# Kernel optimization log

Measured on AMD Instinct MI355X. Metric: run time of the kernel, lower is better.

## Reference

```python
import jax, jax.numpy as jnp
import numpy as np

D = 1024
H = 16
DH = D // H  # 64


def setup_inputs() -> dict:
    key = jax.random.key(0)
    ks = jax.random.split(key, 7)
    X = jax.random.normal(ks[0], (2, 2048, D), dtype=jnp.float32)
    # Per-head projection weights stacked along head axis: [H, D, DH]
    s = 1.0 / np.sqrt(D)
    Wq = jax.random.uniform(ks[1], (H, D, DH), jnp.float32, -s, s)
    Wk = jax.random.uniform(ks[2], (H, D, DH), jnp.float32, -s, s)
    Wv = jax.random.uniform(ks[3], (H, D, DH), jnp.float32, -s, s)
    bq = jax.random.uniform(ks[4], (H, DH), jnp.float32, -s, s)
    bk = jax.random.uniform(ks[5], (H, DH), jnp.float32, -s, s)
    bv = jax.random.uniform(ks[6], (H, DH), jnp.float32, -s, s)
    return {"X": X, "Wq": Wq, "bq": bq, "Wk": Wk, "bk": bk, "Wv": Wv, "bv": bv}


def reference(X, Wq, bq, Wk, bk, Wv, bv):
    B, S, _ = X.shape
    # Per-head linear projections (batched over heads): [B, H, S, DH]
    Q = jnp.einsum('bsd,hde->bhse', X, Wq) + bq[None, :, None, :]
    K = jnp.einsum('bsd,hde->bhse', X, Wk) + bk[None, :, None, :]
    V = jnp.einsum('bsd,hde->bhse', X, Wv) + bv[None, :, None, :]
    scale = jnp.sqrt(jnp.asarray(DH, dtype=X.dtype))
    QK = jnp.einsum('bhse,bhte->bhst', Q, K) / scale  # [B, H, S, S]
    # Faithful to source: softmax over full row FIRST, then lower-tri mask
    # (post-softmax tril, no renormalization).
    sQK = jax.nn.softmax(QK, axis=-1)
    tril = jnp.tril(jnp.ones((S, S), dtype=X.dtype))
    sQK = sQK * tril
    out = jnp.einsum('bhst,bhte->bhse', sQK, V)  # [B, H, S, DH]
    # Concatenate heads along feature dim (torch.cat over per-head outputs)
    return out.transpose(0, 2, 1, 3).reshape(B, S, H * DH)
```

## Files before the change

### kernel.cpp

```cpp
#include <hip/hip_runtime.h>
#include <math.h>

#define B_  2
#define S_  2048
#define D_  1024
#define H_  16
#define DH_ 64

typedef unsigned short u16;
typedef unsigned int   u32;
typedef _Float16       f16;
typedef _Float16 half8  __attribute__((ext_vector_type(8)));
typedef _Float16 half4  __attribute__((ext_vector_type(4)));
typedef float    f32x4  __attribute__((ext_vector_type(4)));

#if __has_builtin(__builtin_amdgcn_exp2f)
#define EXP2(x) __builtin_amdgcn_exp2f(x)
#else
#define EXP2(x) exp2f(x)
#endif

__device__ __forceinline__ u16 h_bits(f16 h){ return __builtin_bit_cast(u16, h); }

__global__ __launch_bounds__(256) void prep_kernel(
    const float* __restrict__ X,
    const float* __restrict__ Wq, const float* __restrict__ Wk,
    const float* __restrict__ Wv,
    u16* __restrict__ Xhi, u16* __restrict__ Xlo, u16* __restrict__ Wt)
{
    __shared__ float Wf[64][65];
    const int bid = blockIdx.x;
    const int c   = threadIdx.x;

    if (bid < 4096){
        const int idx = bid * 256 + c;
        float4 v = ((const float4*)X)[idx];
        float fv[4] = {v.x, v.y, v.z, v.w};
        u16 hh[4], ll[4];
        #pragma unroll
        for (int j = 0; j < 4; ++j){
            f16 hi = (f16)fv[j];
            hh[j] = h_bits(hi);
            ll[j] = h_bits((f16)(fv[j] - (float)hi));
        }
        uint2 ph, pl;
        ph.x = hh[0] | ((u32)hh[1] << 16);
        ph.y = hh[2] | ((u32)hh[3] << 16);
        pl.x = ll[0] | ((u32)ll[1] << 16);
        pl.y = ll[2] | ((u32)ll[3] << 16);
        ((uint2*)Xhi)[idx] = ph;
        ((uint2*)Xlo)[idx] = pl;
        return;
    }

    const int wb = bid - 4096;
    const int d0 = (wb & 15) * 64;
    const int h  = (wb >> 4) & 15;
    const int which = wb >> 8;
    const float* src = (which == 0) ? Wq : (which == 1) ? Wk : Wv;
    src += (size_t)h * D_ * DH_;

    #pragma unroll
    for (int it = 0; it < 4; ++it){
        int d  = (c >> 4) + 16 * it;
        int e4 = (c & 15) * 4;
        float4 v = *(const float4*)(src + (size_t)(d0 + d) * DH_ + e4);
        Wf[d][e4+0] = v.x; Wf[d][e4+1] = v.y; Wf[d][e4+2] = v.z; Wf[d][e4+3] = v.w;
    }
    __syncthreads();
    u16* dst = Wt + (size_t)(which * H_ + h) * DH_ * D_;
    #pragma unroll
    for (int it = 0; it < 4; ++it){
        int e  = (c >> 4) + 16 * it;
        int d4 = (c & 15) * 4;
        u16 q[4];
        #pragma unroll
        for (int j = 0; j < 4; ++j)
            q[j] = h_bits((f16)(Wf[d4 + j][e] * 64.0f));
        u32* p = (u32*)(dst + (size_t)e * D_ + d0 + d4);
        p[0] = q[0] | ((u32)q[1] << 16);
        p[1] = q[2] | ((u32)q[3] << 16);
    }
}

__device__ __forceinline__ void gload16(const void* g, void* l){
    __builtin_amdgcn_global_load_lds(
        (const __attribute__((address_space(1))) void*)g,
        (__attribute__((address_space(3))) void*)l, 16, 0, 0);
}

__device__ __forceinline__ half8 frag16(const char* hb, int row, int quad){
    int off = row * 64 + ((quad * 16) ^ ((row & 6) << 3));
    return __builtin_bit_cast(half8, *(const uint4*)(hb + off));
}

#define FENCE() asm volatile("" ::: "memory")
#define BARX()  do{ FENCE(); __builtin_amdgcn_s_barrier(); FENCE(); }while(0)
#define WAIT_VM4() asm volatile("s_waitcnt vmcnt(4)" ::: "memory")
#define WAIT_VM0() asm volatile("s_waitcnt vmcnt(0)" ::: "memory")

#define STAGE_A(t_, kh_) do{ \
    const int _t = (t_); \
    const int _gk = ((_t & 15) << 6) + ((kh_) << 5); \
    const u16* _g0 = ((_t < 16) ? xa0h : xa0l) + _gk; \
    const u16* _g1 = ((_t < 16) ? xa1h : xa1l) + _gk; \
    char* _l = AsB + ((_t & 1) << 15) + ((kh_) << 14); \
    gload16(_g0, _l + ldw0); \
    gload16(_g1, _l + ldw1); \
}while(0)

#define STAGE_B(t_, kh_) do{ \
    const int _t = (t_); \
    const int _gk = ((_t & 15) << 6) + ((kh_) << 5); \
    char* _l = BsB + ((_t & 1) << 15) + ((kh_) << 14); \
    gload16(wb0 + _gk, _l + ldw0); \
    gload16(wb1 + _gk, _l + ldw1); \
}while(0)

#define READ_B(bh_) do{ \
    _Pragma("unroll") \
    for (int nf_ = 0; nf_ < 4; ++nf_) \
        bfr[nf_] = frag16((bh_), wn * 64 + nf_ * 16 + ln, quad); \
}while(0)

#define READ_A(ah_, mbase_) do{ \
    _Pragma("unroll") \
    for (int mi_ = 0; mi_ < 4; ++mi_) \
        af[mi_] = frag16((ah_), wm * 128 + ((mbase_) + mi_) * 16 + ln, quad); \
}while(0)

#define MFMA_BLOCK(mbase_) do{ \
    BARX(); \
    asm volatile("s_waitcnt lgkmcnt(0)" ::: "memory"); \
    __builtin_amdgcn_sched_barrier(0); \
    __builtin_amdgcn_s_setprio(1); \
    _Pragma("unroll") \
    for (int mi_ = 0; mi_ < 4; ++mi_){ \
        _Pragma("unroll") \
        for (int nf_ = 0; nf_ < 4; ++nf_) \
            acc[(mbase_) + mi_][nf_] = __builtin_amdgcn_mfma_f32_16x16x32_f16( \
                af[mi_], bfr[nf_], acc[(mbase_) + mi_][nf_], 0, 0, 0); \
    } \
    __builtin_amdgcn_s_setprio(0); \
}while(0)

__global__ __launch_bounds__(512, 2) void proj_kernel(
    const u16* __restrict__ Xhi, const u16* __restrict__ Xlo,
    const u16* __restrict__ Wt,
    const float* __restrict__ bq, const float* __restrict__ bk,
    const float* __restrict__ bv,
    f16* __restrict__ Qh, f16* __restrict__ Kh, f16* __restrict__ Vt)
{
    __shared__ __align__(16) char AsB[65536];
    __shared__ __align__(16) char BsB[65536];

    const int tid  = threadIdx.x;
    const int lane = tid & 63;
    const int w    = tid >> 6;
    const int wm   = w >> 2;
    const int wn   = w & 3;
    const int quad = lane >> 4;
    const int ln   = lane & 15;

    const int bid = blockIdx.x;
    const int swz = (bid & 7) * 24 + (bid >> 3);
    const int m0  = (swz / 12) * 256;
    const int c0  = (swz % 12) * 256;

    const int Lr0 = w * 1024 + lane * 16;
    const int Lr1 = (8 + w) * 1024 + lane * 16;
    const int P0  = Lr0 ^ (((Lr0 >> 7) & 3) << 4);
    const int P1  = Lr1 ^ (((Lr1 >> 7) & 3) << 4);
    const int row0 = P0 >> 6,        row1 = P1 >> 6;
    const int ko0  = (P0 & 63) >> 1, ko1  = (P1 & 63) >> 1;

    const u16* xa0h = Xhi + (size_t)(m0 + row0) * D_ + ko0;
    const u16* xa1h = Xhi + (size_t)(m0 + row1) * D_ + ko1;
    const u16* xa0l = Xlo + (size_t)(m0 + row0) * D_ + ko0;
    const u16* xa1l = Xlo + (size_t)(m0 + row1) * D_ + ko1;
    const u16* wb0  = Wt  + (size_t)(c0 + row0) * D_ + ko0;
    const u16* wb1  = Wt  + (size_t)(c0 + row1) * D_ + ko1;

    const int ldw0 = w * 1024;
    const int ldw1 = (8 + w) * 1024;

    f32x4 acc[8][4];
    #pragma unroll
    for (int i = 0; i < 8; ++i)
        #pragma unroll
        for (int j = 0; j < 4; ++j)
            acc[i][j] = (f32x4){0.f, 0.f, 0.f, 0.f};

    STAGE_A(0, 0); STAGE_B(0, 0); STAGE_A(0, 1); STAGE_B(0, 1);
    STAGE_A(1, 0); STAGE_B(1, 0);
    WAIT_VM4();
    BARX();

    half8 bfr[4], af[4];

    #pragma unroll 2
    for (int t = 0; t < 32; ++t){
        const char* Ah = AsB + ((t & 1) << 15);
        const char* Bh = BsB + ((t & 1) << 15);

        READ_B(Bh); READ_A(Ah, 0);
        if (t < 31) STAGE_A(t + 1, 1);
        MFMA_BLOCK(0);
        BARX();

        READ_A(Ah, 4);
        if (t < 31) STAGE_B(t + 1, 1);
        MFMA_BLOCK(4);
        BARX();

        READ_B(Bh + 16384); READ_A(Ah + 16384, 0);
        if (t < 30) STAGE_A(t + 2, 0);
        MFMA_BLOCK(0);
        BARX();

        READ_A(Ah + 16384, 4);
        if (t < 30) STAGE_B(t + 2, 0);
        MFMA_BLOCK(4);
        if (t < 30) { WAIT_VM4(); } else { WAIT_VM0(); }
        BARX();
    }

    const float QSCALE = 0.125f * 1.44269504088896340736f;
    const float INV64  = 0.015625f;
    #pragma unroll
    for (int nf = 0; nf < 4; ++nf){
        int colg  = c0 + wn * 64 + nf * 16 + ln;
        int which = colg >> 10;
        int h     = (colg >> 6) & 15;
        int e     = colg & 63;
        const float* bp = (which == 0) ? bq : (which == 1) ? bk : bv;
        float bias = bp[h * DH_ + e];
        if (which < 2){
            f16* op = (which == 0) ? Qh : Kh;
            float scale = (which == 0) ? QSCALE : 1.0f;
            #pragma unroll
            for (int mf = 0; mf < 8; ++mf)
                #pragma unroll
                for (int r = 0; r < 4; ++r){
                    int sg = m0 + wm * 128 + mf * 16 + 4 * quad + r;
                    int b  = sg >> 11;
                    int s  = sg & (S_ - 1);
                    float val = (acc[mf][nf][r] * INV64 + bias) * scale;
                    op[((size_t)(b * H_ + h) * S_ + s) * DH_ + e] = (f16)val;
                }
        } else {
            #pragma unroll
            for (int mf = 0; mf < 8; ++mf){
                int sg0 = m0 + wm * 128 + mf * 16 + 4 * quad;
                int b   = sg0 >> 11;
                int s0  = sg0 & (S_ - 1);
                u16 p[4];
                #pragma unroll
                for (int r = 0; r < 4; ++r)
                    p[r] = h_bits((f16)(acc[mf][nf][r] * INV64 + bias));
                uint2 pk;
                pk.x = p[0] | ((u32)p[1] << 16);
                pk.y = p[2] | ((u32)p[3] << 16);
                *(uint2*)((u16*)Vt + ((size_t)((b * H_ + h) * DH_ + e)) * S_ + s0) = pk;
            }
        }
    }
}

#define AKS 72

__global__ __launch_bounds__(256, 4) void attn_kernel(
    const f16* __restrict__ Qh, const f16* __restrict__ Kh,
    const f16* __restrict__ Vt, float* __restrict__ Out)
{
    __shared__ u16 Ks[64 * AKS];
    __shared__ u16 Vs[64 * AKS];

    const int tid  = threadIdx.x;
    const int lane = tid & 63;
    const int w    = tid >> 6;
    const int quad = lane >> 4;
    const int ln   = lane & 15;
    const int hb   = blockIdx.x;
    const int i    = blockIdx.y;
    const int h    = hb & 15;
    const int b    = hb >> 4;
    const int bh   = hb;
    const int sub  = w & 1;
    const int qbase = (w >> 1) ? (S_ - 32 * (i + 1) + 16 * sub)
                               : (32 * i + 16 * sub);
    const int vmax  = S_ - 32 * i - 1;

    const u16* Qg = (const u16*)Qh + (size_t)bh * S_ * DH_;
    const u16* Kg = (const u16*)Kh + (size_t)bh * S_ * DH_;
    const u16* Vg = (const u16*)Vt + (size_t)bh * DH_ * S_;

    half8 qf[2];
    #pragma unroll
    for (int ks = 0; ks < 2; ++ks)
        qf[ks] = __builtin_bit_cast(half8,
            *(const uint4*)(Qg + (size_t)(qbase + ln) * DH_ + 32 * ks + 8 * quad));

    const int kr = tid >> 3;
    const int kc = (tid & 7) * 8;

    uint4 kA = *(const uint4*)(Kg + (size_t)kr * DH_ + kc);
    uint4 kB = *(const uint4*)(Kg + (size_t)(kr + 32) * DH_ + kc);
    uint4 vA = *(const uint4*)(Vg + (size_t)kr * S_ + kc);
    uint4 vB = *(const uint4*)(Vg + (size_t)(kr + 32) * S_ + kc);

    float l_r = 0.f;
    f32x4 o_acc[4];
    #pragma unroll
    for (int nt = 0; nt < 4; ++nt) o_acc[nt] = (f32x4){0.f, 0.f, 0.f, 0.f};

    const int qrow   = qbase + ln;
    const int pv_lim = qbase + 15;

    for (int t0 = 0; t0 < S_; t0 += 64){
        __syncthreads();
        *(uint4*)&Ks[kr * AKS + kc]        = kA;
        *(uint4*)&Ks[(kr + 32) * AKS + kc] = kB;
        if (t0 <= vmax){
            *(uint4*)&Vs[kr * AKS + kc]        = vA;
            *(uint4*)&Vs[(kr + 32) * AKS + kc] = vB;
        }
        const int tn = t0 + 64;
        if (tn < S_){
            kA = *(const uint4*)(Kg + (size_t)(tn + kr) * DH_ + kc);
            kB = *(const uint4*)(Kg + (size_t)(tn + kr + 32) * DH_ + kc);
            if (tn <= vmax){
                vA = *(const uint4*)(Vg + (size_t)kr * S_ + tn + kc);
                vB = *(const uint4*)(Vg + (size_t)(kr + 32) * S_ + tn + kc);
            }
        }
        __syncthreads();

        f32x4 sc[4];
        #pragma unroll
        for (int mt = 0; mt < 4; ++mt) sc[mt] = (f32x4){0.f, 0.f, 0.f, 0.f};
        #pragma unroll
        for (int ks = 0; ks < 2; ++ks)
            #pragma unroll
            for (int mt = 0; mt < 4; ++mt){
                half8 kf = __builtin_bit_cast(half8,
                    *(const uint4*)&Ks[(16 * mt + ln) * AKS + 32 * ks + 8 * quad]);
                sc[mt] = __builtin_amdgcn_mfma_f32_16x16x32_f16(kf, qf[ks], sc[mt], 0, 0, 0);
            }

        #pragma unroll
        for (int mt = 0; mt < 4; ++mt)
            #pragma unroll
            for (int r = 0; r < 4; ++r)
                sc[mt][r] = EXP2(sc[mt][r]);
        float s = ((sc[0][0] + sc[0][1] + sc[0][2] + sc[0][3]) +
                   (sc[1][0] + sc[1][1] + sc[1][2] + sc[1][3])) +
                  ((sc[2][0] + sc[2][1] + sc[2][2] + sc[2][3]) +
                   (sc[3][0] + sc[3][1] + sc[3][2] + sc[3][3]));
        s += __shfl_xor(s, 16);
        s += __shfl_xor(s, 32);
        l_r += s;

        #pragma unroll
        for (int mt = 0; mt < 4; ++mt){
            const int ts = t0 + 16 * mt;
            if (ts <= pv_lim){
                half4 pf;
                if (ts == qbase){
                    int tb = ts + 4 * quad;
                    #pragma unroll
                    for (int r = 0; r < 4; ++r)
                        pf[r] = (tb + r > qrow) ? (f16)0.f : (f16)sc[mt][r];
                } else {
                    #pragma unroll
                    for (int r = 0; r < 4; ++r)
                        pf[r] = (f16)sc[mt][r];
                }
                #pragma unroll
                for (int nt = 0; nt < 4; ++nt){
                    half4 vf = __builtin_bit_cast(half4,
                        *(const uint2*)&Vs[(16 * nt + ln) * AKS + 16 * mt + 4 * quad]);
                    o_acc[nt] = __builtin_amdgcn_mfma_f32_16x16x16f16(pf, vf, o_acc[nt], 0, 0, 0);
                }
            }
        }
    }

    #pragma unroll
    for (int r = 0; r < 4; ++r){
        float lv  = __shfl(l_r, (lane & 48) | (4 * quad + r));
        float inv = 1.0f / lv;
        int sg = qbase + 4 * quad + r;
        float* op = Out + ((size_t)b * S_ + sg) * D_ + h * DH_;
        #pragma unroll
        for (int nt = 0; nt < 4; ++nt)
            op[16 * nt + ln] = o_acc[nt][r] * inv;
    }
}

extern "C" void kernel_launch(void* const* d_in, const int* in_sizes, int n_in,
                              void* d_out, int out_size, void* d_ws, size_t ws_size,
                              hipStream_t stream)
{
    const float* X  = (const float*)d_in[0];
    const float* Wq = (const float*)d_in[1];
    const float* bq = (const float*)d_in[2];
    const float* Wk = (const float*)d_in[3];
    const float* bk = (const float*)d_in[4];
    const float* Wv = (const float*)d_in[5];
    const float* bv = (const float*)d_in[6];
    float* out = (float*)d_out;

    u16* Wt  = (u16*)d_ws;
    f16* Qh  = (f16*)(Wt + 3145728);
    f16* Kh  = Qh + 4194304;
    f16* Vt  = Kh + 4194304;
    u16* Xhi = (u16*)(Vt + 4194304);
    u16* Xlo = Xhi + 4194304;

    prep_kernel<<<dim3(4096 + 768), 256, 0, stream>>>(X, Wq, Wk, Wv, Xhi, Xlo, Wt);
    proj_kernel<<<dim3(192), dim3(512), 0, stream>>>(Xhi, Xlo, Wt, bq, bk, bv, Qh, Kh, Vt);
    attn_kernel<<<dim3(32, 32), 256, 0, stream>>>(Qh, Kh, Vt, out);
}
```

Measured before the change: 199.4 us.

## Retile projection GEMM to 256x192 tiles over 256 blocks with register-prefetched fragments

```diff
diff --git a/kernel.cpp b/kernel.cpp
--- a/kernel.cpp
+++ b/kernel.cpp
@@ -94,54 +94,44 @@
     return __builtin_bit_cast(half8, *(const uint4*)(hb + off));
 }
 
-#define FENCE() asm volatile("" ::: "memory")
-#define BARX()  do{ FENCE(); __builtin_amdgcn_s_barrier(); FENCE(); }while(0)
-#define WAIT_VM4() asm volatile("s_waitcnt vmcnt(4)" ::: "memory")
-#define WAIT_VM0() asm volatile("s_waitcnt vmcnt(0)" ::: "memory")
+#define BAR() __builtin_amdgcn_s_barrier()
 
 #define STAGE_A(t_, kh_) do{ \
     const int _t = (t_); \
     const int _gk = ((_t & 15) << 6) + ((kh_) << 5); \
     const u16* _g0 = ((_t < 16) ? xa0h : xa0l) + _gk; \
     const u16* _g1 = ((_t < 16) ? xa1h : xa1l) + _gk; \
-    char* _l = AsB + ((_t & 1) << 15) + ((kh_) << 14); \
+    char* _l = AsB + ((_t & 1) ? 32768 : 0) + ((kh_) << 14); \
     gload16(_g0, _l + ldw0); \
     gload16(_g1, _l + ldw1); \
 }while(0)
 
 #define STAGE_B(t_, kh_) do{ \
-    const int _t = (t_); \
-    const int _gk = ((_t & 15) << 6) + ((kh_) << 5); \
-    char* _l = BsB + ((_t & 1) << 15) + ((kh_) << 14); \
+    const int _gk = (((t_) & 15) << 6) + ((kh_) << 5); \
+    char* _l = BsB + (((t_) & 1) ? 24576 : 0) + ((kh_) ? 12288 : 0); \
     gload16(wb0 + _gk, _l + ldw0); \
-    gload16(wb1 + _gk, _l + ldw1); \
+    if (w < 4) gload16(wb1 + _gk, _l + ldw1); \
 }while(0)
 
-#define READ_B(bh_) do{ \
+#define RD_B(dst_, base_) do{ \
     _Pragma("unroll") \
-    for (int nf_ = 0; nf_ < 4; ++nf_) \
-        bfr[nf_] = frag16((bh_), wn * 64 + nf_ * 16 + ln, quad); \
+    for (int nf_ = 0; nf_ < 3; ++nf_) \
+        dst_[nf_] = frag16((base_), wn * 48 + nf_ * 16 + ln, quad); \
 }while(0)
 
-#define READ_A(ah_, mbase_) do{ \
+#define RD_A(dst_, base_, mo_) do{ \
     _Pragma("unroll") \
     for (int mi_ = 0; mi_ < 4; ++mi_) \
-        af[mi_] = frag16((ah_), wm * 128 + ((mbase_) + mi_) * 16 + ln, quad); \
+        dst_[mi_] = frag16((base_), wm * 128 + (mo_) + mi_ * 16 + ln, quad); \
 }while(0)
 
-#define MFMA_BLOCK(mbase_) do{ \
-    BARX(); \
-    asm volatile("s_waitcnt lgkmcnt(0)" ::: "memory"); \
-    __builtin_amdgcn_sched_barrier(0); \
-    __builtin_amdgcn_s_setprio(1); \
+#define MFMA12(a_, b_, mb_) do{ \
     _Pragma("unroll") \
-    for (int mi_ = 0; mi_ < 4; ++mi_){ \
+    for (int mi_ = 0; mi_ < 4; ++mi_) \
         _Pragma("unroll") \
-        for (int nf_ = 0; nf_ < 4; ++nf_) \
-            acc[(mbase_) + mi_][nf_] = __builtin_amdgcn_mfma_f32_16x16x32_f16( \
-                af[mi_], bfr[nf_], acc[(mbase_) + mi_][nf_], 0, 0, 0); \
-    } \
-    __builtin_amdgcn_s_setprio(0); \
+        for (int nf_ = 0; nf_ < 3; ++nf_) \
+            acc[(mb_) + mi_][nf_] = __builtin_amdgcn_mfma_f32_16x16x32_f16( \
+                a_[mi_], b_[nf_], acc[(mb_) + mi_][nf_], 0, 0, 0); \
 }while(0)
 
 __global__ __launch_bounds__(512, 2) void proj_kernel(
@@ -152,7 +142,7 @@
     f16* __restrict__ Qh, f16* __restrict__ Kh, f16* __restrict__ Vt)
 {
     __shared__ __align__(16) char AsB[65536];
-    __shared__ __align__(16) char BsB[65536];
+    __shared__ __align__(16) char BsB[49152];
 
     const int tid  = threadIdx.x;
     const int lane = tid & 63;
@@ -163,73 +153,88 @@
     const int ln   = lane & 15;
 
     const int bid = blockIdx.x;
-    const int swz = (bid & 7) * 24 + (bid >> 3);
-    const int m0  = (swz / 12) * 256;
-    const int c0  = (swz % 12) * 256;
-
-    const int Lr0 = w * 1024 + lane * 16;
-    const int Lr1 = (8 + w) * 1024 + lane * 16;
-    const int P0  = Lr0 ^ (((Lr0 >> 7) & 3) << 4);
-    const int P1  = Lr1 ^ (((Lr1 >> 7) & 3) << 4);
-    const int row0 = P0 >> 6,        row1 = P1 >> 6;
-    const int ko0  = (P0 & 63) >> 1, ko1  = (P1 & 63) >> 1;
-
-    const u16* xa0h = Xhi + (size_t)(m0 + row0) * D_ + ko0;
-    const u16* xa1h = Xhi + (size_t)(m0 + row1) * D_ + ko1;
-    const u16* xa0l = Xlo + (size_t)(m0 + row0) * D_ + ko0;
-    const u16* xa1l = Xlo + (size_t)(m0 + row1) * D_ + ko1;
-    const u16* wb0  = Wt  + (size_t)(c0 + row0) * D_ + ko0;
-    const u16* wb1  = Wt  + (size_t)(c0 + row1) * D_ + ko1;
+    const int swz = (bid & 7) * 32 + (bid >> 3);
+    const int m0  = (swz >> 4) * 256;
+    const int c0  = (swz & 15) * 192;
+
+    const int Lr0 = tid * 16;
+    const int P0s = Lr0 ^ (((Lr0 >> 7) & 3) << 4);
+    const int rA0 = P0s >> 6;
+    const int ko0 = (P0s & 63) >> 1;
+
+    const u16* xa0h = Xhi + (size_t)(m0 + rA0)       * D_ + ko0;
+    const u16* xa1h = Xhi + (size_t)(m0 + 128 + rA0) * D_ + ko0;
+    const u16* xa0l = Xlo + (size_t)(m0 + rA0)       * D_ + ko0;
+    const u16* xa1l = Xlo + (size_t)(m0 + 128 + rA0) * D_ + ko0;
+    const u16* wb0  = Wt  + (size_t)(c0 + rA0)       * D_ + ko0;
+    const u16* wb1  = Wt  + (size_t)(c0 + 128 + rA0) * D_ + ko0;
 
     const int ldw0 = w * 1024;
-    const int ldw1 = (8 + w) * 1024;
-
-    f32x4 acc[8][4];
+    const int ldw1 = 8192 + w * 1024;
+
+    f32x4 acc[8][3];
     #pragma unroll
     for (int i = 0; i < 8; ++i)
         #pragma unroll
-        for (int j = 0; j < 4; ++j)
+        for (int j = 0; j < 3; ++j)
             acc[i][j] = (f32x4){0.f, 0.f, 0.f, 0.f};
 
     STAGE_A(0, 0); STAGE_B(0, 0); STAGE_A(0, 1); STAGE_B(0, 1);
     STAGE_A(1, 0); STAGE_B(1, 0);
-    WAIT_VM4();
-    BARX();
-
-    half8 bfr[4], af[4];
-
-    #pragma unroll 2
+    asm volatile("s_waitcnt vmcnt(3)" ::: "memory");
+    BAR();
+
+    half8 b0[3], b1[3], a0[4], a1[4], a2[4], a3[4];
+    RD_B(b0, BsB); RD_A(a0, AsB, 0);
+
     for (int t = 0; t < 32; ++t){
-        const char* Ah = AsB + ((t & 1) << 15);
-        const char* Bh = BsB + ((t & 1) << 15);
-
-        READ_B(Bh); READ_A(Ah, 0);
+        const char* Ab = AsB + ((t & 1) ? 32768 : 0);
+        const char* Bb = BsB + ((t & 1) ? 24576 : 0);
+        const char* An = AsB + ((t & 1) ? 0 : 32768);
+        const char* Bn = BsB + ((t & 1) ? 0 : 24576);
+
         if (t < 31) STAGE_A(t + 1, 1);
-        MFMA_BLOCK(0);
-        BARX();
-
-        READ_A(Ah, 4);
+        BAR();
+        __builtin_amdgcn_s_setprio(1);
+        RD_A(a1, Ab, 64);
+        MFMA12(a0, b0, 0);
+        __builtin_amdgcn_s_setprio(0);
+        BAR();
+
         if (t < 31) STAGE_B(t + 1, 1);
-        MFMA_BLOCK(4);
-        BARX();
-
-        READ_B(Bh + 16384); READ_A(Ah + 16384, 0);
+        BAR();
+        __builtin_amdgcn_s_setprio(1);
+        RD_B(b1, Bb + 12288);
+        RD_A(a2, Ab + 16384, 0);
+        MFMA12(a1, b0, 4);
+        __builtin_amdgcn_s_setprio(0);
+        BAR();
+
         if (t < 30) STAGE_A(t + 2, 0);
-        MFMA_BLOCK(0);
-        BARX();
-
-        READ_A(Ah + 16384, 4);
+        BAR();
+        __builtin_amdgcn_s_setprio(1);
+        RD_A(a3, Ab + 16384, 64);
+        MFMA12(a2, b1, 0);
+        __builtin_amdgcn_s_setprio(0);
+        BAR();
+
         if (t < 30) STAGE_B(t + 2, 0);
-        MFMA_BLOCK(4);
-        if (t < 30) { WAIT_VM4(); } else { WAIT_VM0(); }
-        BARX();
+        if (t < 30) { asm volatile("s_waitcnt vmcnt(3)" ::: "memory"); }
+        else        { asm volatile("s_waitcnt vmcnt(0)" ::: "memory"); }
+        BAR();
+        __builtin_amdgcn_s_setprio(1);
+        RD_B(b0, Bn);
+        RD_A(a0, An, 0);
+        MFMA12(a3, b1, 4);
+        __builtin_amdgcn_s_setprio(0);
+        BAR();
     }
 
     const float QSCALE = 0.125f * 1.44269504088896340736f;
     const float INV64  = 0.015625f;
     #pragma unroll
-    for (int nf = 0; nf < 4; ++nf){
-        int colg  = c0 + wn * 64 + nf * 16 + ln;
+    for (int nf = 0; nf < 3; ++nf){
+        int colg  = c0 + wn * 48 + nf * 16 + ln;
         int which = colg >> 10;
         int h     = (colg >> 6) & 15;
         int e     = colg & 63;
@@ -419,6 +424,6 @@
     u16* Xlo = Xhi + 4194304;
 
     prep_kernel<<<dim3(4096 + 768), 256, 0, stream>>>(X, Wq, Wk, Wv, Xhi, Xlo, Wt);
-    proj_kernel<<<dim3(192), dim3(512), 0, stream>>>(Xhi, Xlo, Wt, bq, bk, bv, Qh, Kh, Vt);
+    proj_kernel<<<dim3(256), dim3(512), 0, stream>>>(Xhi, Xlo, Wt, bq, bk, bv, Qh, Kh, Vt);
     attn_kernel<<<dim3(32, 32), 256, 0, stream>>>(Qh, Kh, Vt, out);
 }
```

Result: faster. 194.1 us (-2.6%).
